# Kernel tuning notes

Measured on AMD Instinct MI355X. Metric: run time of the kernel, lower is better.

Reference implementation:

```python
import jax, jax.numpy as jnp
import numpy as np
import math

B, L, D = 8, 2048, 1024
DK = D  # self.dk = input_size


def setup_inputs() -> dict:
    key = jax.random.key(0)
    ks = jax.random.split(key, 7)
    s = 1.0 / math.sqrt(D)
    return {
        "x": jax.random.normal(ks[0], (B, L, D), jnp.float32),
        "queries": jax.random.normal(ks[1], (B, L, D), jnp.float32),
        "values": jax.random.normal(ks[2], (B, L, D), jnp.float32),
        "attention_mask": jnp.ones((B, L), jnp.float32),
        "Wk": jax.random.normal(ks[3], (D, D), jnp.float32) * s,
        "Wq_self": jax.random.normal(ks[4], (D, D), jnp.float32) * s,
        "Wq_other": jax.random.normal(ks[5], (D, D), jnp.float32) * s,
        "Wv": jax.random.normal(ks[6], (D, D), jnp.float32) * s,
    }


def reference(x, queries, values, attention_mask, Wk, Wq_self, Wq_other, Wv):
    # nn.Linear(bias=False): y = x @ W.T, weight W is [out, in]
    k = jnp.einsum('bld,ad->bla', x, Wk)
    q_s = jnp.einsum('bld,ad->bla', x, Wq_self)
    q_o = jnp.einsum('bld,ad->bla', queries, Wq_other)
    v = jnp.einsum('bld,ad->bla', values, Wv)

    scale = 1.0 / math.sqrt(DK)
    penalty = (1.0 - attention_mask)[:, None, :] * -100000.0  # (B,1,L)

    scores_self = jnp.einsum('bqa,bka->bqk', q_s, k) * scale + penalty
    scores_other = jnp.einsum('bqa,bka->bqk', q_o, k) * scale + penalty

    p_self = jax.nn.softmax(scores_self, axis=-1)   # dropout is eval/no-op
    p_other = jax.nn.softmax(scores_other, axis=-1)

    out = jnp.einsum('bqk,bka->bqa', p_self, v) + jnp.einsum('bqk,bka->bqa', p_other, v)
    return out, p_self
```

## Files before the change

### kernel.cpp

```cpp
#include <hip/hip_runtime.h>
#include <hip/hip_bf16.h>
#include <cstdint>
#include <cstddef>


#define B_ 8
#define L_ 2048
#define D_ 1024

typedef __attribute__((ext_vector_type(8))) short short8;
typedef __attribute__((ext_vector_type(4))) float floatx4;

__device__ __forceinline__ ushort f2bf(float f) {
  union { float f; uint32_t u; } v; v.f = f;
  return (ushort)((v.u + 0x7FFFu + ((v.u >> 16) & 1u)) >> 16);
}
__device__ __forceinline__ float bf2f(ushort u) {
  union { uint32_t u; float f; } v; v.u = ((uint32_t)u) << 16;
  return v.f;
}

__device__ __forceinline__ void gload_lds16(const ushort* g, ushort* l) {
  __builtin_amdgcn_global_load_lds(
      (const __attribute__((address_space(1))) void*)g,
      (__attribute__((address_space(3))) void*)l, 16, 0, 0);
}

template<int MODE>
__global__ __launch_bounds__(256) void gemm_bt(
    const ushort* __restrict__ A, long long aBatch, int aStride,
    const ushort* __restrict__ Bm, long long bBatch, int bStride,
    void* __restrict__ Cv, long long cBatch, int cStride,
    int K, const float* __restrict__ mask, float scale)
{
  __shared__ alignas(16) ushort lA[2][128 * 32];
  __shared__ alignas(16) ushort lB[2][128 * 32];
  const int tid  = threadIdx.x;
  const int lane = tid & 63;
  const int wave = tid >> 6;
  const int z    = blockIdx.z;

  int asel = z, bsel = z, msel = 0;
  if (MODE == 0) { asel = (z & 1) + (z == 3); }
  if (MODE == 1) { bsel = z & 7; msel = z & 7; }

  const ushort* Ab = A + (long long)asel * aBatch + (long long)blockIdx.x * 128 * aStride;
  const ushort* Bb = Bm + (long long)bsel * bBatch + (long long)blockIdx.y * 128 * bStride;

  const int wm = (wave & 1) * 64;
  const int wn = (wave >> 1) * 64;

  const floatx4 zero = {0.f, 0.f, 0.f, 0.f};
  floatx4 acc[4][4];
#pragma unroll
  for (int i = 0; i < 4; i++)
#pragma unroll
    for (int j = 0; j < 4; j++) acc[i][j] = zero;

  const int srow = tid >> 2;
  const int scol = (tid & 3) << 3;

  for (int k0 = 0; k0 < K; k0 += 64) {
    __syncthreads();
#pragma unroll
    for (int h = 0; h < 2; ++h) {
#pragma unroll
      for (int j = 0; j < 2; ++j) {
        int row = srow + j * 64;
        int l   = (j * 256 + tid) * 8;
        gload_lds16(Ab + (long long)row * aStride + (k0 + h * 32 + scol), lA[h] + l);
        gload_lds16(Bb + (long long)row * bStride + (k0 + h * 32 + scol), lB[h] + l);
      }
    }
    __syncthreads();

#pragma unroll
    for (int h = 0; h < 2; ++h) {
      short8 af[4], bg[4];
#pragma unroll
      for (int i = 0; i < 4; i++) {
        af[i] = *(const short8*)(lA[h] + ((wm + i * 16 + (lane & 15)) * 32 + (lane >> 4) * 8));
        bg[i] = *(const short8*)(lB[h] + ((wn + i * 16 + (lane & 15)) * 32 + (lane >> 4) * 8));
      }
#pragma unroll
      for (int i = 0; i < 4; i++)
#pragma unroll
        for (int j = 0; j < 4; j++)
          acc[i][j] = __builtin_amdgcn_mfma_f32_16x16x32_bf16(af[i], bg[j], acc[i][j], 0, 0, 0);
    }
  }

  const int m0 = blockIdx.x * 128 + wm + (lane >> 4) * 4;
  const int n0 = blockIdx.y * 128 + wn + (lane & 15);

  if (MODE == 2) {
    float* C = (float*)Cv + (long long)z * cBatch;
#pragma unroll
    for (int i = 0; i < 4; i++)
#pragma unroll
      for (int j = 0; j < 4; j++)
#pragma unroll
        for (int r = 0; r < 4; r++)
          C[(long long)(m0 + i * 16 + r) * cStride + (n0 + j * 16)] = acc[i][j][r];
  } else {
    ushort* C = (ushort*)Cv + (long long)z * cBatch;
#pragma unroll
    for (int j = 0; j < 4; j++) {
      const int gc = n0 + j * 16;
      float pen = 0.f;
      if (MODE == 1) pen = (1.0f - mask[(long long)msel * L_ + gc]) * -100000.0f;
#pragma unroll
      for (int i = 0; i < 4; i++)
#pragma unroll
        for (int r = 0; r < 4; r++) {
          float v = acc[i][j][r];
          if (MODE == 1) v = v * scale + pen;
          C[(long long)(m0 + i * 16 + r) * cStride + gc] = f2bf(v);
        }
    }
  }
}

__global__ __launch_bounds__(256) void transpose_bf16(
    const ushort* __restrict__ V, ushort* __restrict__ Vt)
{
  __shared__ ushort t[64][66];
  const int b = blockIdx.z;
  const int k0 = blockIdx.x * 64;
  const int a0 = blockIdx.y * 64;
  const ushort* Vb = V + (size_t)b * (L_ * D_);
  ushort* Vtb = Vt + (size_t)b * (D_ * L_);
  const int tx = threadIdx.x & 63;
  const int ty = threadIdx.x >> 6;
#pragma unroll
  for (int r = 0; r < 16; ++r) {
    int row = r * 4 + ty;
    t[row][tx] = Vb[(size_t)(k0 + row) * D_ + (a0 + tx)];
  }
  __syncthreads();
#pragma unroll
  for (int r = 0; r < 16; ++r) {
    int row = r * 4 + ty;
    Vtb[(size_t)(a0 + row) * L_ + (k0 + tx)] = t[tx][row];
  }
}

__device__ __forceinline__ float block_red(float v, bool domax, float* red)
{
#pragma unroll
  for (int off = 32; off > 0; off >>= 1) {
    float o = __shfl_xor(v, off, 64);
    v = domax ? fmaxf(v, o) : (v + o);
  }
  __syncthreads();
  if ((threadIdx.x & 63) == 0) red[threadIdx.x >> 6] = v;
  __syncthreads();
  return domax ? fmaxf(fmaxf(red[0], red[1]), fmaxf(red[2], red[3]))
               : (red[0] + red[1] + red[2] + red[3]);
}

__global__ __launch_bounds__(256) void softmax2(
    const ushort* __restrict__ S, float* __restrict__ pself)
{
  __shared__ float red[4];
  const size_t row = blockIdx.x;
  const int tid = threadIdx.x;
  const size_t half = (size_t)B_ * L_ * L_;

  const uint4* rs = (const uint4*)(S + row * L_);
  const uint4* ro = (const uint4*)(S + half + row * L_);
  uint4 us = rs[tid];
  uint4 uo = ro[tid];

  float vs[8], vo[8];
  const ushort* ps = (const ushort*)&us;
  const ushort* po = (const ushort*)&uo;
#pragma unroll
  for (int j = 0; j < 8; j++) { vs[j] = bf2f(ps[j]); vo[j] = bf2f(po[j]); }

  float ms = -3.0e38f, mo = -3.0e38f;
#pragma unroll
  for (int j = 0; j < 8; j++) { ms = fmaxf(ms, vs[j]); mo = fmaxf(mo, vo[j]); }
  ms = block_red(ms, true, red);
  mo = block_red(mo, true, red);

  float ss = 0.f, so = 0.f;
#pragma unroll
  for (int j = 0; j < 8; j++) {
    vs[j] = __expf(vs[j] - ms); ss += vs[j];
    vo[j] = __expf(vo[j] - mo); so += vo[j];
  }
  ss = block_red(ss, false, red);
  so = block_red(so, false, red);
  const float is = 1.f / ss, io = 1.f / so;

  float* pr = pself + row * (size_t)L_ + (size_t)tid * 8;
  float4 o0, o1;
  o0.x = vs[0] * is; o0.y = vs[1] * is; o0.z = vs[2] * is; o0.w = vs[3] * is;
  o1.x = vs[4] * is; o1.y = vs[5] * is; o1.z = vs[6] * is; o1.w = vs[7] * is;
  ((float4*)pr)[0] = o0;
  ((float4*)pr)[1] = o1;

  uint4 up;
  ushort* pp = (ushort*)&up;
#pragma unroll
  for (int j = 0; j < 8; j++) pp[j] = f2bf(vs[j] * is + vo[j] * io);
  ((uint4*)(S + half + row * L_))[tid] = up;
}

__global__ __launch_bounds__(256) void cvt4(
    const float* __restrict__ s0, const float* __restrict__ s1,
    const float* __restrict__ s2, const float* __restrict__ s3,
    ushort* __restrict__ dst, int n4)
{
  const float* s = (blockIdx.z == 0) ? s0 : (blockIdx.z == 1) ? s1
                   : (blockIdx.z == 2) ? s2 : s3;
  ushort* d = dst + (size_t)blockIdx.z * (size_t)n4 * 4;
  const float4* sv = (const float4*)s;
  ushort4* dv = (ushort4*)d;
  for (int i = blockIdx.x * 256 + threadIdx.x; i < n4; i += gridDim.x * 256) {
    float4 f = sv[i];
    ushort4 o; o.x = f2bf(f.x); o.y = f2bf(f.y); o.z = f2bf(f.z); o.w = f2bf(f.w);
    dv[i] = o;
  }
}

extern "C" void kernel_launch(void* const* d_in, const int* in_sizes, int n_in,
                              void* d_out, int out_size, void* d_ws, size_t ws_size,
                              hipStream_t stream)
{
  const float* x    = (const float*)d_in[0];
  const float* qry  = (const float*)d_in[1];
  const float* val  = (const float*)d_in[2];
  const float* mask = (const float*)d_in[3];
  const float* Wk   = (const float*)d_in[4];
  const float* Wqs  = (const float*)d_in[5];
  const float* Wqo  = (const float*)d_in[6];
  const float* Wv   = (const float*)d_in[7];

  const size_t NE = (size_t)B_ * L_ * D_;
  const size_t NW = (size_t)D_ * D_;
  const size_t NS = (size_t)B_ * L_ * L_;

  float*  out   = (float*)d_out;
  float*  pself = out + NE;

  ushort* ob = (ushort*)d_out;
  ushort* Qs   = ob;
  ushort* Qo   = ob + NE;
  ushort* Kb   = ob + 2 * NE;
  ushort* Vtmp = ob + 3 * NE;

  char* ws = (char*)d_ws;
  ushort* xb = (ushort*)ws;
  ushort* W4 = xb + 3 * NE;
  ushort* Sc = (ushort*)ws;
  ushort* Psum = Sc + NS;
  ushort* Vt = (ushort*)(ws + (size_t)134217728);

  const float scale = 0.03125f;

  cvt4<<<dim3(4096, 1, 3), 256, 0, stream>>>(x, qry, val, nullptr, xb, (int)(NE / 4));
  cvt4<<<dim3(1024, 1, 4), 256, 0, stream>>>(Wqs, Wqo, Wk, Wv, W4, (int)(NW / 4));

  gemm_bt<0><<<dim3(128, 8, 4), 256, 0, stream>>>(
      xb, (long long)NE, D_, W4, (long long)NW, D_,
      ob, (long long)NE, D_, D_, nullptr, 1.f);

  transpose_bf16<<<dim3(L_ / 64, D_ / 64, B_), 256, 0, stream>>>(Vtmp, Vt);

  gemm_bt<1><<<dim3(16, 16, 16), 256, 0, stream>>>(
      Qs, (long long)L_ * D_, D_, Kb, (long long)L_ * D_, D_,
      Sc, (long long)L_ * L_, L_, D_, mask, scale);

  softmax2<<<dim3(B_ * L_, 1, 1), 256, 0, stream>>>(Sc, pself);

  gemm_bt<2><<<dim3(16, 8, 8), 256, 0, stream>>>(
      Psum, (long long)L_ * L_, L_, Vt, (long long)D_ * L_, L_,
      out, (long long)L_ * D_, D_, L_, nullptr, 1.f);
}
```

Baseline: 901.1 us.

## Replace GEMM with 256x256 8-wave pipelined kernel using swizzled LDS and XCD remap

Replaces the 128x128, 4-wave bf16 GEMM with a 256x256 tile, 8-wave kernel using 64-wide K slices. Global-to-LDS loads are double-buffered and interleaved with MFMA phases under explicit barriers and waitcnts. The LDS layout is XOR-swizzled to avoid bank conflicts. Block IDs are remapped across XCDs for cache locality. This aims to raise data reuse and hide load latency, at the cost of much higher register and LDS pressure and fragile hand-written synchronisation.

```diff
diff --git a/kernel.cpp b/kernel.cpp
--- a/kernel.cpp
+++ b/kernel.cpp
@@ -26,94 +26,162 @@
       (__attribute__((address_space(3))) void*)l, 16, 0, 0);
 }
 
+__device__ __forceinline__ void stage_half(
+    const ushort* __restrict__ g, int stride, ushort* lds, int tid)
+{
+#pragma unroll
+  for (int p = 0; p < 2; ++p) {
+    const int grow  = p * 64 + (tid >> 3);
+    const int gslot = (tid & 7) ^ (grow & 7);
+    gload_lds16(g + grow * stride + gslot * 8, lds + p * 4096 + tid * 8);
+  }
+}
+
+__device__ __forceinline__ short8 ldfrag(const ushort* L, int row, int g) {
+  return *(const short8*)(L + row * 64 + ((g ^ (row & 7)) << 3));
+}
+
+#define MFMA_ __builtin_amdgcn_mfma_f32_16x16x32_bf16
+
+#define PHASE(bufp, ks, nh, DOA, STAGE_BLOCK, WAIT_BLOCK) do {               \
+    if (DOA) {                                                               \
+      const ushort* LA_ = lA[bufp];                                          \
+      _Pragma("unroll")                                                      \
+      for (int i_ = 0; i_ < 8; ++i_)                                         \
+        af[i_] = ldfrag(LA_, wr * 128 + i_ * 16 + lan15, (ks) * 4 + lan4);   \
+    }                                                                        \
+    {                                                                        \
+      const ushort* LB_ = lB[bufp];                                          \
+      const int rb_ = wc * 64 + (nh) * 32 + lan15;                           \
+      bf0 = ldfrag(LB_, rb_,      (ks) * 4 + lan4);                          \
+      bf1 = ldfrag(LB_, rb_ + 16, (ks) * 4 + lan4);                          \
+    }                                                                        \
+    STAGE_BLOCK;                                                             \
+    asm volatile("" ::: "memory");                                           \
+    __builtin_amdgcn_s_barrier();                                            \
+    asm volatile("s_waitcnt lgkmcnt(0)" ::: "memory");                       \
+    __builtin_amdgcn_sched_barrier(0);                                       \
+    __builtin_amdgcn_s_setprio(1);                                           \
+    _Pragma("unroll")                                                        \
+    for (int i_ = 0; i_ < 8; ++i_) {                                         \
+      acc[i_][(nh) * 2]     = MFMA_(af[i_], bf0, acc[i_][(nh) * 2],     0, 0, 0); \
+      acc[i_][(nh) * 2 + 1] = MFMA_(af[i_], bf1, acc[i_][(nh) * 2 + 1], 0, 0, 0); \
+    }                                                                        \
+    __builtin_amdgcn_s_setprio(0);                                           \
+    WAIT_BLOCK;                                                              \
+    asm volatile("" ::: "memory");                                           \
+    __builtin_amdgcn_s_barrier();                                            \
+    asm volatile("" ::: "memory");                                           \
+  } while (0)
+
 template<int MODE>
-__global__ __launch_bounds__(256) void gemm_bt(
+__global__ __launch_bounds__(512, 2) void gemm8(
     const ushort* __restrict__ A, long long aBatch, int aStride,
     const ushort* __restrict__ Bm, long long bBatch, int bStride,
     void* __restrict__ Cv, long long cBatch, int cStride,
     int K, const float* __restrict__ mask, float scale)
 {
-  __shared__ alignas(16) ushort lA[2][128 * 32];
-  __shared__ alignas(16) ushort lB[2][128 * 32];
-  const int tid  = threadIdx.x;
-  const int lane = tid & 63;
-  const int wave = tid >> 6;
-  const int z    = blockIdx.z;
-
-  int asel = z, bsel = z, msel = 0;
-  if (MODE == 0) { asel = (z & 1) + (z == 3); }
-  if (MODE == 1) { bsel = z & 7; msel = z & 7; }
-
-  const ushort* Ab = A + (long long)asel * aBatch + (long long)blockIdx.x * 128 * aStride;
-  const ushort* Bb = Bm + (long long)bsel * bBatch + (long long)blockIdx.y * 128 * bStride;
-
-  const int wm = (wave & 1) * 64;
-  const int wn = (wave >> 1) * 64;
+  __shared__ alignas(16) ushort lA[2][256 * 64];
+  __shared__ alignas(16) ushort lB[2][256 * 64];
+
+  const int tid   = threadIdx.x;
+  const int lane  = tid & 63;
+  const int wave  = tid >> 6;
+  const int wr    = wave >> 2;
+  const int wc    = wave & 3;
+  const int lan15 = lane & 15;
+  const int lan4  = lane >> 4;
+
+  const unsigned gx = gridDim.x, gy = gridDim.y;
+  unsigned f = blockIdx.x + gx * (blockIdx.y + gy * blockIdx.z);
+  const unsigned nwg = gx * gy * gridDim.z;
+  f = (f & 7) * (nwg >> 3) + (f >> 3);
+  const int bx = f % gx;
+  const int by = (f / gx) % gy;
+  const int bz = f / (gx * gy);
+
+  int asel = bz, bsel = bz, msel = 0;
+  if (MODE == 0) { asel = (bz & 1) + (bz == 3); }
+  if (MODE == 1) { bsel = bz & 7; msel = bz & 7; }
+
+  const ushort* Ab = A  + (long long)asel * aBatch + (long long)bx * 256 * aStride;
+  const ushort* Bb = Bm + (long long)bsel * bBatch + (long long)by * 256 * bStride;
 
   const floatx4 zero = {0.f, 0.f, 0.f, 0.f};
-  floatx4 acc[4][4];
-#pragma unroll
-  for (int i = 0; i < 4; i++)
+  floatx4 acc[8][4];
+#pragma unroll
+  for (int i = 0; i < 8; i++)
 #pragma unroll
     for (int j = 0; j < 4; j++) acc[i][j] = zero;
 
-  const int srow = tid >> 2;
-  const int scol = (tid & 3) << 3;
-
-  for (int k0 = 0; k0 < K; k0 += 64) {
-    __syncthreads();
-#pragma unroll
-    for (int h = 0; h < 2; ++h) {
-#pragma unroll
-      for (int j = 0; j < 2; ++j) {
-        int row = srow + j * 64;
-        int l   = (j * 256 + tid) * 8;
-        gload_lds16(Ab + (long long)row * aStride + (k0 + h * 32 + scol), lA[h] + l);
-        gload_lds16(Bb + (long long)row * bStride + (k0 + h * 32 + scol), lB[h] + l);
-      }
-    }
-    __syncthreads();
-
-#pragma unroll
-    for (int h = 0; h < 2; ++h) {
-      short8 af[4], bg[4];
-#pragma unroll
-      for (int i = 0; i < 4; i++) {
-        af[i] = *(const short8*)(lA[h] + ((wm + i * 16 + (lane & 15)) * 32 + (lane >> 4) * 8));
-        bg[i] = *(const short8*)(lB[h] + ((wn + i * 16 + (lane & 15)) * 32 + (lane >> 4) * 8));
-      }
-#pragma unroll
-      for (int i = 0; i < 4; i++)
-#pragma unroll
-        for (int j = 0; j < 4; j++)
-          acc[i][j] = __builtin_amdgcn_mfma_f32_16x16x32_bf16(af[i], bg[j], acc[i][j], 0, 0, 0);
-    }
-  }
-
-  const int m0 = blockIdx.x * 128 + wm + (lane >> 4) * 4;
-  const int n0 = blockIdx.y * 128 + wn + (lane & 15);
+  const int NT  = K >> 6;
+  const int NIT = NT >> 1;
+
+  stage_half(Ab,                      aStride, &lA[0][0],    tid);
+  stage_half(Ab + 128 * aStride,      aStride, &lA[0][8192], tid);
+  stage_half(Bb,                      bStride, &lB[0][0],    tid);
+  stage_half(Bb + 128 * bStride,      bStride, &lB[0][8192], tid);
+  stage_half(Ab + 64,                 aStride, &lA[1][0],    tid);
+  stage_half(Ab + 128 * aStride + 64, aStride, &lA[1][8192], tid);
+  asm volatile("s_waitcnt vmcnt(4)" ::: "memory");
+  __builtin_amdgcn_s_barrier();
+  asm volatile("" ::: "memory");
+
+  short8 af[8], bf0, bf1;
+
+  for (int it = 0; it < NIT; ++it) {
+    const int  t2   = it * 2;
+    const bool full = (it < NIT - 1);
+    const int  kB1  = (t2 + 1) << 6;
+    const int  kA2  = (t2 + 2) << 6;
+    const int  kA3  = (t2 + 3) << 6;
+
+    PHASE(0, 0, 0, true,
+          { stage_half(Bb + kB1, bStride, &lB[1][0], tid); }, {});
+    PHASE(0, 0, 1, false,
+          { stage_half(Bb + 128 * bStride + kB1, bStride, &lB[1][8192], tid); }, {});
+    PHASE(0, 1, 0, true, {}, {});
+    PHASE(0, 1, 1, false,
+          { if (full) stage_half(Ab + kA2, aStride, &lA[0][0], tid); },
+          { if (full) { asm volatile("s_waitcnt vmcnt(2)" ::: "memory"); }
+            else      { asm volatile("s_waitcnt vmcnt(0)" ::: "memory"); } });
+
+    PHASE(1, 0, 0, true,
+          { if (full) stage_half(Ab + 128 * aStride + kA2, aStride, &lA[0][8192], tid); }, {});
+    PHASE(1, 0, 1, false,
+          { if (full) stage_half(Bb + kA2, bStride, &lB[0][0], tid); }, {});
+    PHASE(1, 1, 0, true,
+          { if (full) stage_half(Bb + 128 * bStride + kA2, bStride, &lB[0][8192], tid); }, {});
+    PHASE(1, 1, 1, false,
+          { if (full) { stage_half(Ab + kA3, aStride, &lA[1][0], tid);
+                        stage_half(Ab + 128 * aStride + kA3, aStride, &lA[1][8192], tid); } },
+          { if (full) { asm volatile("s_waitcnt vmcnt(4)" ::: "memory"); } });
+  }
+
+  const int m0 = bx * 256 + wr * 128 + (lane >> 4) * 4;
+  const int n0 = by * 256 + wc * 64 + (lane & 15);
 
   if (MODE == 2) {
-    float* C = (float*)Cv + (long long)z * cBatch;
-#pragma unroll
-    for (int i = 0; i < 4; i++)
-#pragma unroll
-      for (int j = 0; j < 4; j++)
+    float* C = (float*)Cv + (long long)bz * cBatch;
+#pragma unroll
+    for (int i = 0; i < 8; i++)
+#pragma unroll
+      for (int n = 0; n < 4; n++)
 #pragma unroll
         for (int r = 0; r < 4; r++)
-          C[(long long)(m0 + i * 16 + r) * cStride + (n0 + j * 16)] = acc[i][j][r];
+          C[(long long)(m0 + i * 16 + r) * cStride + (n0 + n * 16)] = acc[i][n][r];
   } else {
-    ushort* C = (ushort*)Cv + (long long)z * cBatch;
-#pragma unroll
-    for (int j = 0; j < 4; j++) {
-      const int gc = n0 + j * 16;
+    ushort* C = (ushort*)Cv + (long long)bz * cBatch;
+#pragma unroll
+    for (int n = 0; n < 4; n++) {
+      const int gc = n0 + n * 16;
       float pen = 0.f;
       if (MODE == 1) pen = (1.0f - mask[(long long)msel * L_ + gc]) * -100000.0f;
 #pragma unroll
-      for (int i = 0; i < 4; i++)
+      for (int i = 0; i < 8; i++)
 #pragma unroll
         for (int r = 0; r < 4; r++) {
-          float v = acc[i][j][r];
+          float v = acc[i][n][r];
           if (MODE == 1) v = v * scale + pen;
           C[(long long)(m0 + i * 16 + r) * cStride + gc] = f2bf(v);
         }
@@ -263,19 +331,19 @@
   cvt4<<<dim3(4096, 1, 3), 256, 0, stream>>>(x, qry, val, nullptr, xb, (int)(NE / 4));
   cvt4<<<dim3(1024, 1, 4), 256, 0, stream>>>(Wqs, Wqo, Wk, Wv, W4, (int)(NW / 4));
 
-  gemm_bt<0><<<dim3(128, 8, 4), 256, 0, stream>>>(
+  gemm8<0><<<dim3(64, 4, 4), 512, 0, stream>>>(
       xb, (long long)NE, D_, W4, (long long)NW, D_,
       ob, (long long)NE, D_, D_, nullptr, 1.f);
 
   transpose_bf16<<<dim3(L_ / 64, D_ / 64, B_), 256, 0, stream>>>(Vtmp, Vt);
 
-  gemm_bt<1><<<dim3(16, 16, 16), 256, 0, stream>>>(
+  gemm8<1><<<dim3(8, 8, 16), 512, 0, stream>>>(
       Qs, (long long)L_ * D_, D_, Kb, (long long)L_ * D_, D_,
       Sc, (long long)L_ * L_, L_, D_, mask, scale);
 
   softmax2<<<dim3(B_ * L_, 1, 1), 256, 0, stream>>>(Sc, pself);
 
-  gemm_bt<2><<<dim3(16, 8, 8), 256, 0, stream>>>(
+  gemm8<2><<<dim3(8, 4, 8), 512, 0, stream>>>(
       Psum, (long long)L_ * L_, L_, Vt, (long long)D_ * L_, L_,
       out, (long long)L_ * D_, D_, L_, nullptr, 1.f);
 }
```

Result: slower. 1.004 ms (+11.4%).
